# Kernel tuning notes

Measured on AMD Instinct MI355X. Metric: run time of the kernel, lower is better.

The kernel has to match this reference:

```python
import jax, jax.numpy as jnp
import numpy as np

B, P, N, M = 8, 50, 128, 128          # batch, pomo, query nodes, route tokens
EMB, H, D = 128, 8, 16                # embedding_dim, head_num, qkv_dim
NE, K = 8, 2                          # num_experts, top-k
CLIP = 10.0                           # logit_clipping


def setup_inputs() -> dict:
    key = jax.random.key(0)
    ks = jax.random.split(key, 12)
    s = 0.02
    return {
        "encoded_nodes": jax.random.normal(ks[0], (B, P, N, EMB), jnp.float32),
        "encoded_routes": jax.random.normal(ks[1], (B, P, M, EMB + 1), jnp.float32),
        "ninf_mask": jnp.zeros((B, P, N), jnp.float32),
        "route_mask": jnp.zeros((B, P, N, M), jnp.float32),
        "Wq": s * jax.random.normal(ks[2], (EMB, H * D), jnp.float32),
        "Wk": s * jax.random.normal(ks[3], (EMB + 1, H * D), jnp.float32),
        "Wv": s * jax.random.normal(ks[4], (EMB + 1, H * D), jnp.float32),
        "Wg": s * jax.random.normal(ks[5], (H * D, NE), jnp.float32),
        "We": s * jax.random.normal(ks[6], (NE, H * D, EMB + 1), jnp.float32),
        "be": jnp.zeros((NE, EMB + 1), jnp.float32),
        "Wfinal": s * jax.random.normal(ks[7], (EMB + 1, 1), jnp.float32),
    }


def _heads(x, W):
    # x: [B,P,n,F] @ W[F,H*D] -> [B,P,H,n,D]
    y = x @ W
    b, p, n, _ = y.shape
    return jnp.swapaxes(y.reshape(b, p, n, H, D), 2, 3)


def reference(encoded_nodes, encoded_routes, ninf_mask, route_mask,
              Wq, Wk, Wv, Wg, We, be, Wfinal):
    # --- masked multi-head attention (multi_head_attention1) ---
    q = _heads(encoded_nodes, Wq)          # [B,P,H,N,D]
    k = _heads(encoded_routes, Wk)         # [B,P,H,M,D]
    v = _heads(encoded_routes, Wv)         # [B,P,H,M,D]
    score = jnp.einsum('bphnd,bphmd->bphnm', q, k) / jnp.sqrt(jnp.float32(D))
    score = score + route_mask[:, :, None, :, :]          # rank3 ninf mask
    w = jax.nn.softmax(score, axis=-1)
    # rank2 mask applied multiplicatively after softmax
    keep = jnp.where(ninf_mask == 0.0, 1.0, 0.0)[:, :, None, :, None]
    w = w * keep
    out = jnp.einsum('bphnm,bphmd->bphnd', w, v)
    out_concat = jnp.swapaxes(out, 2, 3).reshape(B, P, N, H * D)

    # --- top-k gated MoE combine (noisy gating, eval: no noise) ---
    x = out_concat.reshape(-1, H * D)                     # [T, H*D]
    T = x.shape[0]
    gate_logits = x @ Wg                                  # [T, NE]
    top_vals, top_idx = jax.lax.top_k(gate_logits, K)
    top_g = jax.nn.softmax(top_vals, axis=-1)
    gates = jnp.zeros((T, NE), x.dtype).at[jnp.arange(T)[:, None], top_idx].set(top_g)
    expert_out = jnp.einsum('ti,eio->teo', x, We) + be    # [T, NE, EMB+1]
    moe_out = jnp.einsum('te,teo->to', gates, expert_out)
    importance = gates.sum(0)
    moe_loss = importance.var() / (importance.mean() ** 2 + 1e-10)
    mh_atten_out = moe_out.reshape(B, P, N, EMB + 1)

    # --- final scoring ---
    score_scaled = (mh_atten_out @ Wfinal)[..., 0]        # [B,P,N]
    score_clipped = CLIP * jnp.tanh(score_scaled)
    score_masked = score_clipped + ninf_mask
    probs = jax.nn.softmax(score_masked, axis=2)
    return probs, moe_loss
```

## Files before the change

### kernel.cpp

```cpp
#include <hip/hip_runtime.h>

constexpr int B  = 8,  P = 50, N = 128, M = 128;
constexpr int EMB = 128, H = 8, D = 16;
constexpr int NE = 8;
constexpr int HD = H * D;
constexpr int E1 = EMB + 1;
constexpr int BP = B * P;
constexpr int T  = BP * N;

__global__ void prep_kernel(const float* __restrict__ We,
                            const float* __restrict__ be,
                            const float* __restrict__ Wf,
                            float* __restrict__ Wep, float* __restrict__ bpv,
                            float* __restrict__ importance,
                            unsigned* __restrict__ ticket) {
    const int e = blockIdx.x;
    const int f = threadIdx.x;

    float a = 0.f;
    const long base = ((long)e * HD + f) * E1;
    for (int o = 0; o < E1; ++o) a += We[base + o] * Wf[o];
    Wep[e * HD + f] = a;

    if (f == 0) {
        float b = 0.f;
        for (int o = 0; o < E1; ++o) b += be[(long)e * E1 + o] * Wf[o];
        bpv[e] = b;
    }
    if (e == 0 && f < NE) importance[f] = 0.f;
    if (e == 0 && f == NE) *ticket = 0u;
}

__global__ __launch_bounds__(256) void proj_kernel(
    const float* __restrict__ nodes,
    const float* __restrict__ routes,
    const float* __restrict__ Wq, const float* __restrict__ Wk,
    const float* __restrict__ Wv,
    float* __restrict__ qo, float* __restrict__ ko, float* __restrict__ vo) {
    const int mat = blockIdx.y;
    const float* __restrict__ X = (mat == 0) ? nodes : routes;
    const float* __restrict__ W = (mat == 0) ? Wq : (mat == 1 ? Wk : Wv);
    float* __restrict__ out     = (mat == 0) ? qo : (mat == 1 ? ko : vo);
    const int Kd = (mat == 0) ? EMB : E1;
    const int nit = (Kd + 7) >> 3;

    const int row0 = blockIdx.x * 128;
    const int tid  = threadIdx.x;
    const int tr   = tid >> 4;
    const int tc   = tid & 15;

    __shared__ float XT[2][8][132];
    __shared__ float WS[2][8][132];

    float acc[8][8];
    #pragma unroll
    for (int i = 0; i < 8; ++i)
        #pragma unroll
        for (int j = 0; j < 8; ++j) acc[i][j] = 0.f;

    float xr[4];
    float4 wr;
    const int xkx = tid & 7, xrr = tid >> 3;
    const int wkx = tid >> 5, wc4 = (tid & 31) * 4;

    {
        #pragma unroll
        for (int i = 0; i < 4; ++i) {
            int kg = xkx;
            xr[i] = (kg < Kd) ? X[(long)(row0 + xrr + i * 32) * Kd + kg] : 0.f;
        }
        wr = (wkx < Kd) ? *(const float4*)&W[(long)wkx * HD + wc4]
                        : make_float4(0.f, 0.f, 0.f, 0.f);
        #pragma unroll
        for (int i = 0; i < 4; ++i) XT[0][xkx][xrr + i * 32] = xr[i];
        *(float4*)&WS[0][wkx][wc4] = wr;
    }
    __syncthreads();

    for (int it = 0; it < nit; ++it) {
        const int buf = it & 1;
        if (it + 1 < nit) {
            const int kk = (it + 1) * 8;
            #pragma unroll
            for (int i = 0; i < 4; ++i) {
                int kg = kk + xkx;
                xr[i] = (kg < Kd) ? X[(long)(row0 + xrr + i * 32) * Kd + kg] : 0.f;
            }
            int kg = kk + wkx;
            wr = (kg < Kd) ? *(const float4*)&W[(long)kg * HD + wc4]
                           : make_float4(0.f, 0.f, 0.f, 0.f);
        }

        #pragma unroll
        for (int k = 0; k < 8; ++k) {
            float4 xa = *(const float4*)&XT[buf][k][tr * 4];
            float4 xb = *(const float4*)&XT[buf][k][64 + tr * 4];
            float4 wa = *(const float4*)&WS[buf][k][tc * 4];
            float4 wb = *(const float4*)&WS[buf][k][64 + tc * 4];
            float xv[8] = {xa.x, xa.y, xa.z, xa.w, xb.x, xb.y, xb.z, xb.w};
            float wvv[8] = {wa.x, wa.y, wa.z, wa.w, wb.x, wb.y, wb.z, wb.w};
            #pragma unroll
            for (int i = 0; i < 8; ++i)
                #pragma unroll
                for (int j = 0; j < 8; ++j) acc[i][j] += xv[i] * wvv[j];
        }

        if (it + 1 < nit) {
            const int nb = buf ^ 1;
            #pragma unroll
            for (int i = 0; i < 4; ++i) XT[nb][xkx][xrr + i * 32] = xr[i];
            *(float4*)&WS[nb][wkx][wc4] = wr;
        }
        __syncthreads();
    }

    #pragma unroll
    for (int i = 0; i < 8; ++i) {
        int r = row0 + (i < 4 ? 0 : 64) + tr * 4 + (i & 3);
        float4 o0 = make_float4(acc[i][0], acc[i][1], acc[i][2], acc[i][3]);
        float4 o1 = make_float4(acc[i][4], acc[i][5], acc[i][6], acc[i][7]);
        *(float4*)&out[(long)r * HD + tc * 4]      = o0;
        *(float4*)&out[(long)r * HD + 64 + tc * 4] = o1;
    }
}

__global__ __launch_bounds__(64) void attn_kernel(
    const float* __restrict__ qbuf,
    const float* __restrict__ kbuf,
    const float* __restrict__ vbuf,
    const float* __restrict__ rmask,
    const float* __restrict__ ninf,
    float* __restrict__ xcat) {
    const int bp  = blockIdx.x;
    const int h   = blockIdx.y;
    const int tid = threadIdx.x;

    __shared__ float kh[M][D];

    #pragma unroll
    for (int i = 0; i < 8; ++i) {
        int e = tid + i * 64;
        int r = e >> 2, c4 = (e & 3) * 4;
        *(float4*)&kh[r][c4] = *(const float4*)&kbuf[((long)bp * M + r) * HD + h * D + c4];
    }
    __syncthreads();

    const long t0 = (long)bp * N + tid, t1 = t0 + 64;

    float qr0[16], qr1[16];
    {
        const float4* q0 = (const float4*)&qbuf[t0 * HD + h * D];
        const float4* q1 = (const float4*)&qbuf[t1 * HD + h * D];
        #pragma unroll
        for (int i = 0; i < 4; ++i) {
            float4 a = q0[i], b = q1[i];
            qr0[i*4+0] = a.x*0.25f; qr0[i*4+1] = a.y*0.25f;
            qr0[i*4+2] = a.z*0.25f; qr0[i*4+3] = a.w*0.25f;
            qr1[i*4+0] = b.x*0.25f; qr1[i*4+1] = b.y*0.25f;
            qr1[i*4+2] = b.z*0.25f; qr1[i*4+3] = b.w*0.25f;
        }
    }

    const float* __restrict__ vbase = vbuf + ((long)bp * M) * HD + h * D;
    const float4* rm0 = (const float4*)&rmask[t0 * M];
    const float4* rm1 = (const float4*)&rmask[t1 * M];

    float sum0 = 0.f, sum1 = 0.f;
    float o0[16], o1[16];
    #pragma unroll
    for (int d = 0; d < 16; ++d) { o0[d] = 0.f; o1[d] = 0.f; }

    float4 a0 = rm0[0], a1 = rm1[0];
    float4 b0 = rm0[1], b1 = rm1[1];

    for (int mb = 0; mb < 32; ++mb) {
        const int mn = (mb + 2 < 32) ? (mb + 2) : 31;
        float4 c0 = rm0[mn], c1 = rm1[mn];
        float r0v[4] = {a0.x, a0.y, a0.z, a0.w};
        float r1v[4] = {a1.x, a1.y, a1.z, a1.w};
        #pragma unroll
        for (int j = 0; j < 4; ++j) {
            const int m = mb * 4 + j;
            const float4* k4 = (const float4*)&kh[m][0];
            const float4* v4 = (const float4*)&vbase[(long)m * HD];
            float s0 = 0.f, s1 = 0.f;
            #pragma unroll
            for (int q4 = 0; q4 < 4; ++q4) {
                float4 kq = k4[q4];
                s0 += qr0[q4*4+0]*kq.x + qr0[q4*4+1]*kq.y
                    + qr0[q4*4+2]*kq.z + qr0[q4*4+3]*kq.w;
                s1 += qr1[q4*4+0]*kq.x + qr1[q4*4+1]*kq.y
                    + qr1[q4*4+2]*kq.z + qr1[q4*4+3]*kq.w;
            }
            float e0 = __expf(s0 + r0v[j]);
            float e1 = __expf(s1 + r1v[j]);
            sum0 += e0; sum1 += e1;
            #pragma unroll
            for (int q4 = 0; q4 < 4; ++q4) {
                float4 vq = v4[q4];
                o0[q4*4+0] += e0*vq.x; o0[q4*4+1] += e0*vq.y;
                o0[q4*4+2] += e0*vq.z; o0[q4*4+3] += e0*vq.w;
                o1[q4*4+0] += e1*vq.x; o1[q4*4+1] += e1*vq.y;
                o1[q4*4+2] += e1*vq.z; o1[q4*4+3] += e1*vq.w;
            }
        }
        a0 = b0; a1 = b1; b0 = c0; b1 = c1;
    }

    const float inv0 = ((ninf[t0] == 0.f) ? 1.f : 0.f) / sum0;
    const float inv1 = ((ninf[t1] == 0.f) ? 1.f : 0.f) / sum1;
    #pragma unroll
    for (int q4 = 0; q4 < 4; ++q4) {
        float4 w0 = make_float4(o0[q4*4+0]*inv0, o0[q4*4+1]*inv0,
                                o0[q4*4+2]*inv0, o0[q4*4+3]*inv0);
        float4 w1 = make_float4(o1[q4*4+0]*inv1, o1[q4*4+1]*inv1,
                                o1[q4*4+2]*inv1, o1[q4*4+3]*inv1);
        *(float4*)&xcat[t0 * HD + h * D + q4 * 4] = w0;
        *(float4*)&xcat[t1 * HD + h * D + q4 * 4] = w1;
    }
}

__global__ __launch_bounds__(128) void moe_final_kernel(
    const float* __restrict__ xcat, const float* __restrict__ Wg,
    const float* __restrict__ ninf, const float* __restrict__ Wep,
    const float* __restrict__ bpv, float* __restrict__ importance,
    unsigned* __restrict__ ticket, float* __restrict__ out) {
    __shared__ float WgS[EMB][NE];
    __shared__ float WeS[NE][132];
    __shared__ float red[N];
    __shared__ float impS[NE];

    const int bp = blockIdx.x;
    const int n  = threadIdx.x;

    #pragma unroll
    for (int i = 0; i < 2; ++i) {
        int e = n + i * 128;
        int r = e >> 1, c4 = (e & 1) * 4;
        *(float4*)&WgS[r][c4] = *(const float4*)&Wg[(long)r * NE + c4];
    }
    #pragma unroll
    for (int i = 0; i < 2; ++i) {
        int idx = n + i * 128;
        int r = idx >> 5, c = (idx & 31) * 4;
        *(float4*)&WeS[r][c] = *(const float4*)&Wep[(long)r * HD + c];
    }
    if (n < NE) impS[n] = 0.f;
    __syncthreads();

    const long t = (long)bp * N + n;
    const float4* row4 = (const float4*)&xcat[t * HD];

    float gl[NE];
    #pragma unroll
    for (int e = 0; e < NE; ++e) gl[e] = 0.f;
    for (int fb = 0; fb < 32; ++fb) {
        float4 xv = row4[fb];
        float x4[4] = {xv.x, xv.y, xv.z, xv.w};
        #pragma unroll
        for (int j = 0; j < 4; ++j)
            #pragma unroll
            for (int e = 0; e < NE; ++e) gl[e] += x4[j] * WgS[fb * 4 + j][e];
    }

    int e0 = 0; float v0 = gl[0];
    #pragma unroll
    for (int e = 1; e < NE; ++e) if (gl[e] > v0) { v0 = gl[e]; e0 = e; }
    int e1 = -1; float v1 = -3.4e38f;
    #pragma unroll
    for (int e = 0; e < NE; ++e) if (e != e0 && gl[e] > v1) { v1 = gl[e]; e1 = e; }
    float ex = __expf(v1 - v0);
    float g0 = 1.f / (1.f + ex);
    float g1 = ex / (1.f + ex);

    atomicAdd(&impS[e0], g0);
    atomicAdd(&impS[e1], g1);

    float s = g0 * bpv[e0] + g1 * bpv[e1];
    for (int fb = 0; fb < 32; ++fb) {
        float4 xv = row4[fb];
        float x4[4] = {xv.x, xv.y, xv.z, xv.w};
        #pragma unroll
        for (int j = 0; j < 4; ++j) {
            int f = fb * 4 + j;
            s += x4[j] * (g0 * WeS[e0][f] + g1 * WeS[e1][f]);
        }
    }
    s = 10.f * tanhf(s) + ninf[t];

    red[n] = s;
    __syncthreads();
    for (int off = 64; off > 0; off >>= 1) {
        if (n < off) red[n] = fmaxf(red[n], red[n + off]);
        __syncthreads();
    }
    float mx = red[0];
    __syncthreads();
    float e = __expf(s - mx);
    red[n] = e;
    __syncthreads();
    for (int off = 64; off > 0; off >>= 1) {
        if (n < off) red[n] += red[n + off];
        __syncthreads();
    }
    float sum = red[0];

    out[t] = e / sum;

    if (n < NE) atomicAdd(&importance[n], impS[n]);

    __syncthreads();
    if (n == 0) {
        __threadfence();
        unsigned tk = atomicAdd(ticket, 1u);
        if (tk == BP - 1) {
            __threadfence();
            float imp[NE];
            #pragma unroll
            for (int ei = 0; ei < NE; ++ei)
                imp[ei] = atomicAdd(&importance[ei], 0.f);
            float mean = 0.f;
            #pragma unroll
            for (int ei = 0; ei < NE; ++ei) mean += imp[ei];
            mean *= (1.f / NE);
            float var = 0.f;
            #pragma unroll
            for (int ei = 0; ei < NE; ++ei) {
                float d = imp[ei] - mean;
                var += d * d;
            }
            var *= (1.f / NE);
            out[T] = var / (mean * mean + 1e-10f);
        }
    }
}

extern "C" void kernel_launch(void* const* d_in, const int* in_sizes, int n_in,
                              void* d_out, int out_size, void* d_ws, size_t ws_size,
                              hipStream_t stream) {
    const float* nodes  = (const float*)d_in[0];
    const float* routes = (const float*)d_in[1];
    const float* ninf   = (const float*)d_in[2];
    const float* rmask  = (const float*)d_in[3];
    const float* Wq     = (const float*)d_in[4];
    const float* Wk     = (const float*)d_in[5];
    const float* Wv     = (const float*)d_in[6];
    const float* Wg     = (const float*)d_in[7];
    const float* We     = (const float*)d_in[8];
    const float* be     = (const float*)d_in[9];
    const float* Wfin   = (const float*)d_in[10];

    float* ws = (float*)d_ws;
    float* Wep        = ws + 16;
    float* bpv        = ws + 1040;
    float* importance = ws + 1048;
    unsigned* ticket  = (unsigned*)(ws + 1056);
    float* qbuf       = ws + 4096;
    float* kbuf       = qbuf + (long)T * HD;
    float* vbuf       = kbuf + (long)T * HD;
    float* xcat       = vbuf + (long)T * HD;

    float* out = (float*)d_out;

    prep_kernel<<<NE, 128, 0, stream>>>(We, be, Wfin, Wep, bpv, importance,
                                        ticket);
    proj_kernel<<<dim3(400, 3), 256, 0, stream>>>(nodes, routes, Wq, Wk, Wv,
                                                  qbuf, kbuf, vbuf);
    attn_kernel<<<dim3(BP, H), 64, 0, stream>>>(qbuf, kbuf, vbuf,
                                                rmask, ninf, xcat);
    moe_final_kernel<<<BP, 128, 0, stream>>>(xcat, Wg, ninf, Wep, bpv,
                                             importance, ticket, out);
}
```

Measured before the change: 300.6 us.

## Fold prep into proj launch and store attention output feature-major for MoE

The separate prep kernel is merged into the projection kernel as an extra grid row, which removes one launch. The attention kernel now writes its output transposed (feature-major per bp), so the MoE kernel's per-token reads across threads become coalesced scalar loads instead of strided float4 row reads. The manual route-mask register prefetch in the attention loop is dropped in favour of direct loads. The trade-offs are 392 idle blocks in the extended grid and scalar, non-vectorized stores from attention.

Result: faster. 286.1 us, median of 3 (-4.8%).

```diff
diff --git a/kernel.cpp b/kernel.cpp
--- a/kernel.cpp
+++ b/kernel.cpp
@@ -8,36 +8,39 @@
 constexpr int BP = B * P;
 constexpr int T  = BP * N;
 
-__global__ void prep_kernel(const float* __restrict__ We,
-                            const float* __restrict__ be,
-                            const float* __restrict__ Wf,
-                            float* __restrict__ Wep, float* __restrict__ bpv,
-                            float* __restrict__ importance,
-                            unsigned* __restrict__ ticket) {
-    const int e = blockIdx.x;
-    const int f = threadIdx.x;
-
-    float a = 0.f;
-    const long base = ((long)e * HD + f) * E1;
-    for (int o = 0; o < E1; ++o) a += We[base + o] * Wf[o];
-    Wep[e * HD + f] = a;
-
-    if (f == 0) {
-        float b = 0.f;
-        for (int o = 0; o < E1; ++o) b += be[(long)e * E1 + o] * Wf[o];
-        bpv[e] = b;
-    }
-    if (e == 0 && f < NE) importance[f] = 0.f;
-    if (e == 0 && f == NE) *ticket = 0u;
-}
-
 __global__ __launch_bounds__(256) void proj_kernel(
     const float* __restrict__ nodes,
     const float* __restrict__ routes,
     const float* __restrict__ Wq, const float* __restrict__ Wk,
     const float* __restrict__ Wv,
-    float* __restrict__ qo, float* __restrict__ ko, float* __restrict__ vo) {
+    float* __restrict__ qo, float* __restrict__ ko, float* __restrict__ vo,
+    const float* __restrict__ We, const float* __restrict__ be,
+    const float* __restrict__ Wf,
+    float* __restrict__ Wep, float* __restrict__ bpv,
+    float* __restrict__ importance, unsigned* __restrict__ ticket) {
     const int mat = blockIdx.y;
+
+    if (mat == 3) {
+        const int e = blockIdx.x;
+        if (e >= NE) return;
+        const int f = threadIdx.x;
+        if (f < HD) {
+            float a = 0.f;
+            const long base = ((long)e * HD + f) * E1;
+            for (int o = 0; o < E1; ++o) a += We[base + o] * Wf[o];
+            Wep[e * HD + f] = a;
+        } else if (f == HD) {
+            float b = 0.f;
+            for (int o = 0; o < E1; ++o) b += be[(long)e * E1 + o] * Wf[o];
+            bpv[e] = b;
+        }
+        if (e == 0) {
+            if (f >= 140 && f < 140 + NE) importance[f - 140] = 0.f;
+            if (f == 150) *ticket = 0u;
+        }
+        return;
+    }
+
     const float* __restrict__ X = (mat == 0) ? nodes : routes;
     const float* __restrict__ W = (mat == 0) ? Wq : (mat == 1 ? Wk : Wv);
     float* __restrict__ out     = (mat == 0) ? qo : (mat == 1 ? ko : vo);
@@ -130,7 +133,7 @@
     const float* __restrict__ vbuf,
     const float* __restrict__ rmask,
     const float* __restrict__ ninf,
-    float* __restrict__ xcat) {
+    float* __restrict__ xcatT) {
     const int bp  = blockIdx.x;
     const int h   = blockIdx.y;
     const int tid = threadIdx.x;
@@ -170,14 +173,10 @@
     #pragma unroll
     for (int d = 0; d < 16; ++d) { o0[d] = 0.f; o1[d] = 0.f; }
 
-    float4 a0 = rm0[0], a1 = rm1[0];
-    float4 b0 = rm0[1], b1 = rm1[1];
-
     for (int mb = 0; mb < 32; ++mb) {
-        const int mn = (mb + 2 < 32) ? (mb + 2) : 31;
-        float4 c0 = rm0[mn], c1 = rm1[mn];
-        float r0v[4] = {a0.x, a0.y, a0.z, a0.w};
-        float r1v[4] = {a1.x, a1.y, a1.z, a1.w};
+        float4 r0 = rm0[mb], r1 = rm1[mb];
+        float r0v[4] = {r0.x, r0.y, r0.z, r0.w};
+        float r1v[4] = {r1.x, r1.y, r1.z, r1.w};
         #pragma unroll
         for (int j = 0; j < 4; ++j) {
             const int m = mb * 4 + j;
@@ -204,24 +203,21 @@
                 o1[q4*4+2] += e1*vq.z; o1[q4*4+3] += e1*vq.w;
             }
         }
-        a0 = b0; a1 = b1; b0 = c0; b1 = c1;
     }
 
     const float inv0 = ((ninf[t0] == 0.f) ? 1.f : 0.f) / sum0;
     const float inv1 = ((ninf[t1] == 0.f) ? 1.f : 0.f) / sum1;
-    #pragma unroll
-    for (int q4 = 0; q4 < 4; ++q4) {
-        float4 w0 = make_float4(o0[q4*4+0]*inv0, o0[q4*4+1]*inv0,
-                                o0[q4*4+2]*inv0, o0[q4*4+3]*inv0);
-        float4 w1 = make_float4(o1[q4*4+0]*inv1, o1[q4*4+1]*inv1,
-                                o1[q4*4+2]*inv1, o1[q4*4+3]*inv1);
-        *(float4*)&xcat[t0 * HD + h * D + q4 * 4] = w0;
-        *(float4*)&xcat[t1 * HD + h * D + q4 * 4] = w1;
+    float* __restrict__ xb = xcatT + (long)bp * HD * N + (long)h * D * N;
+    #pragma unroll
+    for (int d = 0; d < 16; ++d) {
+        xb[d * N + tid]      = o0[d] * inv0;
+        xb[d * N + tid + 64] = o1[d] * inv1;
     }
 }
 
 __global__ __launch_bounds__(128) void moe_final_kernel(
-    const float* __restrict__ xcat, const float* __restrict__ Wg,
+    const float* __restrict__ xcatT,
+    const float* __restrict__ Wg,
     const float* __restrict__ ninf, const float* __restrict__ Wep,
     const float* __restrict__ bpv, float* __restrict__ importance,
     unsigned* __restrict__ ticket, float* __restrict__ out) {
@@ -249,18 +245,15 @@
     __syncthreads();
 
     const long t = (long)bp * N + n;
-    const float4* row4 = (const float4*)&xcat[t * HD];
+    const float* __restrict__ xrow = xcatT + (long)bp * HD * N;
 
     float gl[NE];
     #pragma unroll
     for (int e = 0; e < NE; ++e) gl[e] = 0.f;
-    for (int fb = 0; fb < 32; ++fb) {
-        float4 xv = row4[fb];
-        float x4[4] = {xv.x, xv.y, xv.z, xv.w};
-        #pragma unroll
-        for (int j = 0; j < 4; ++j)
-            #pragma unroll
-            for (int e = 0; e < NE; ++e) gl[e] += x4[j] * WgS[fb * 4 + j][e];
+    for (int f = 0; f < HD; ++f) {
+        float xv = xrow[f * N + n];
+        #pragma unroll
+        for (int e = 0; e < NE; ++e) gl[e] += xv * WgS[f][e];
     }
 
     int e0 = 0; float v0 = gl[0];
@@ -277,14 +270,9 @@
     atomicAdd(&impS[e1], g1);
 
     float s = g0 * bpv[e0] + g1 * bpv[e1];
-    for (int fb = 0; fb < 32; ++fb) {
-        float4 xv = row4[fb];
-        float x4[4] = {xv.x, xv.y, xv.z, xv.w};
-        #pragma unroll
-        for (int j = 0; j < 4; ++j) {
-            int f = fb * 4 + j;
-            s += x4[j] * (g0 * WeS[e0][f] + g1 * WeS[e1][f]);
-        }
+    for (int f = 0; f < HD; ++f) {
+        float xv = xrow[f * N + n];
+        s += xv * (g0 * WeS[e0][f] + g1 * WeS[e1][f]);
     }
     s = 10.f * tanhf(s) + ninf[t];
 
@@ -358,16 +346,16 @@
     float* qbuf       = ws + 4096;
     float* kbuf       = qbuf + (long)T * HD;
     float* vbuf       = kbuf + (long)T * HD;
-    float* xcat       = vbuf + (long)T * HD;
+    float* xcatT      = vbuf + (long)T * HD;
 
     float* out = (float*)d_out;
 
-    prep_kernel<<<NE, 128, 0, stream>>>(We, be, Wfin, Wep, bpv, importance,
-                                        ticket);
-    proj_kernel<<<dim3(400, 3), 256, 0, stream>>>(nodes, routes, Wq, Wk, Wv,
-                                                  qbuf, kbuf, vbuf);
+    proj_kernel<<<dim3(400, 4), 256, 0, stream>>>(nodes, routes, Wq, Wk, Wv,
+                                                  qbuf, kbuf, vbuf,
+                                                  We, be, Wfin, Wep, bpv,
+                                                  importance, ticket);
     attn_kernel<<<dim3(BP, H), 64, 0, stream>>>(qbuf, kbuf, vbuf,
-                                                rmask, ninf, xcat);
-    moe_final_kernel<<<BP, 128, 0, stream>>>(xcat, Wg, ninf, Wep, bpv,
+                                                rmask, ninf, xcatT);
+    moe_final_kernel<<<BP, 128, 0, stream>>>(xcatT, Wg, ninf, Wep, bpv,
                                              importance, ticket, out);
 }
```
